# Optimization experiments

Measured on AMD Instinct MI355X. Metric: run time of the kernel, lower is better.

## Reference

```python
import jax, jax.numpy as jnp
import numpy as np
import math

B, S, E, H = 2, 2048, 1024, 16
D = E // H  # head_dim = 64


def setup_inputs() -> dict:
    key = jax.random.key(0)
    ks = jax.random.split(key, 12)
    scale = 1.0 / math.sqrt(E)
    inp = {
        "q": jax.random.normal(ks[0], (B, S, E), jnp.float32),
        "k": jax.random.normal(ks[1], (B, S, E), jnp.float32),
        "v": jax.random.normal(ks[2], (B, S, E), jnp.float32),
        # causal mask, broadcast over batch and heads
        "mask": jnp.tril(jnp.ones((S, S), jnp.bool_))[None, None, :, :],
        "Wq": jax.random.normal(ks[3], (E, E), jnp.float32) * scale,
        "bq": jnp.zeros((E,), jnp.float32),
        "Wk": jax.random.normal(ks[4], (E, E), jnp.float32) * scale,
        "bk": jnp.zeros((E,), jnp.float32),
        "Wv": jax.random.normal(ks[5], (E, E), jnp.float32) * scale,
        "bv": jnp.zeros((E,), jnp.float32),
        "Wo": jax.random.normal(ks[6], (E, E), jnp.float32) * scale,
        "bo": jnp.zeros((E,), jnp.float32),
    }
    return inp


def _heads(x, W, b):
    # nn.Linear: x @ W.T + b, then split into heads -> [B, H, S, D]
    y = x @ W.T + b
    return y.reshape(B, S, H, D).transpose(0, 2, 1, 3)


def reference(q, k, v, mask, Wq, bq, Wk, bk, Wv, bv, Wo, bo):
    qh = _heads(q, Wq, bq)   # [B,H,S,D]
    kh = _heads(k, Wk, bk)
    vh = _heads(v, Wv, bv)
    scores = jnp.einsum("bhqd,bhkd->bhqk", qh, kh) / math.sqrt(D)
    scores = jnp.where(mask, scores, -1e9)
    probs = jax.nn.softmax(scores, axis=-1)  # dropout is identity in eval
    ctx = jnp.einsum("bhqk,bhkd->bhqd", probs, vh)
    ctx = ctx.transpose(0, 2, 1, 3).reshape(B, S, E)
    return ctx @ Wo.T + bo
```

## Files before the change

### kernel.cpp

```cpp
#include <hip/hip_runtime.h>
#include <hip/hip_bf16.h>
#include <cstdint>

#define PB 2
#define PS 2048
#define PE 1024
#define PH 16
#define PD 64

typedef __attribute__((ext_vector_type(8))) short short8;
typedef __attribute__((ext_vector_type(8))) ushort u16x8;
typedef __attribute__((ext_vector_type(4))) float f32x4;

static __device__ __forceinline__ float bf2f(ushort u) {
  return __uint_as_float(((unsigned)u) << 16);
}
static __device__ __forceinline__ ushort f2bf(float f) {
  unsigned u = __float_as_uint(f);
  u += 0x7fffu + ((u >> 16) & 1u);
  return (ushort)(u >> 16);
}

static __device__ __forceinline__ void async16(void* lds, const void* g) {
  __attribute__((address_space(3))) unsigned* l =
      reinterpret_cast<__attribute__((address_space(3))) unsigned*>(
          reinterpret_cast<uintptr_t>(lds));
  const __attribute__((address_space(1))) unsigned* gp =
      reinterpret_cast<const __attribute__((address_space(1))) unsigned*>(
          reinterpret_cast<uintptr_t>(g));
  __builtin_amdgcn_global_load_lds(gp, l, 16, 0, 0);
}

__global__ __launch_bounds__(256)
void cvt_kernel(const float* __restrict__ s0, const float* __restrict__ s1,
                const float* __restrict__ s2, const float* __restrict__ s3,
                const float* __restrict__ s4, const float* __restrict__ s5,
                const float* __restrict__ s6,
                ushort* d0, ushort* d1, ushort* d2, ushort* d3, ushort* d4,
                ushort* d5, ushort* d6) {
  const int t = blockIdx.y;
  const float* src = t == 0 ? s0 : t == 1 ? s1 : t == 2 ? s2 : t == 3 ? s3
                   : t == 4 ? s4 : t == 5 ? s5 : s6;
  ushort* dst = t == 0 ? d0 : t == 1 ? d1 : t == 2 ? d2 : t == 3 ? d3
              : t == 4 ? d4 : t == 5 ? d5 : d6;
  const size_t n = (t < 3) ? (size_t)4194304 : (size_t)1048576;
  const size_t i0 = ((size_t)blockIdx.x * 256 + threadIdx.x) * 8;
  if (i0 >= n) return;
  const f32x4 a = *(const f32x4*)(src + i0);
  const f32x4 b = *(const f32x4*)(src + i0 + 4);
  u16x8 o;
  o[0] = f2bf(a[0]); o[1] = f2bf(a[1]); o[2] = f2bf(a[2]); o[3] = f2bf(a[3]);
  o[4] = f2bf(b[0]); o[5] = f2bf(b[1]); o[6] = f2bf(b[2]); o[7] = f2bf(b[3]);
  *(u16x8*)(dst + i0) = o;
}

template <bool SWAP>
__device__ __forceinline__ void gemm_core(const ushort* __restrict__ A,
                                          const ushort* __restrict__ W,
                                          int m0, int n0,
                                          ushort* As, ushort* Bs,
                                          f32x4 acc[4][4]) {
  const int tid  = threadIdx.x;
  const int wave = tid >> 6;
  const int lane = tid & 63;
  const int quad = lane >> 4;
  const int lrow = lane & 15;
  const int wm = wave >> 1;
  const int wn = wave & 1;
  const int row0 = tid >> 2;
  const int kc8  = (tid & 3) * 8;

  for (int kt = 0; kt < PE; kt += 32) {
    async16(As + (size_t)wave * 512,        A + (size_t)(m0 + row0)      * PE + kt + kc8);
    async16(As + 2048 + (size_t)wave * 512, A + (size_t)(m0 + row0 + 64) * PE + kt + kc8);
    async16(Bs + (size_t)wave * 512,        W + (size_t)(n0 + row0)      * PE + kt + kc8);
    async16(Bs + 2048 + (size_t)wave * 512, W + (size_t)(n0 + row0 + 64) * PE + kt + kc8);
    __syncthreads();
    short8 af[4], bf[4];
#pragma unroll
    for (int i = 0; i < 4; ++i) {
      af[i] = *(const short8*)(As + (wm * 64 + i * 16 + lrow) * 32 + quad * 8);
      bf[i] = *(const short8*)(Bs + (wn * 64 + i * 16 + lrow) * 32 + quad * 8);
    }
#pragma unroll
    for (int i = 0; i < 4; ++i)
#pragma unroll
      for (int j = 0; j < 4; ++j) {
        if (SWAP)
          acc[i][j] = __builtin_amdgcn_mfma_f32_16x16x32_bf16(bf[j], af[i], acc[i][j], 0, 0, 0);
        else
          acc[i][j] = __builtin_amdgcn_mfma_f32_16x16x32_bf16(af[i], bf[j], acc[i][j], 0, 0, 0);
      }
    __syncthreads();
  }
}

__global__ __launch_bounds__(256)
void qkv_kernel(const ushort* __restrict__ q, const ushort* __restrict__ k,
                const ushort* __restrict__ v,
                const ushort* __restrict__ Wq, const ushort* __restrict__ Wk,
                const ushort* __restrict__ Wv,
                const float* __restrict__ bq, const float* __restrict__ bk,
                const float* __restrict__ bv,
                ushort* __restrict__ qh, ushort* __restrict__ kh,
                ushort* __restrict__ vt) {
  __shared__ __align__(16) ushort As[128 * 32];
  __shared__ __align__(16) ushort Bs[128 * 32];
  const int which = blockIdx.x >> 3;
  const int n0 = (blockIdx.x & 7) * 128;
  const int m0 = blockIdx.y * 128;
  const ushort* A  = which == 0 ? q  : (which == 1 ? k  : v);
  const ushort* W  = which == 0 ? Wq : (which == 1 ? Wk : Wv);
  const float* bi  = which == 0 ? bq : (which == 1 ? bk : bv);

  const int lane = threadIdx.x & 63;
  const int wave = threadIdx.x >> 6;
  const int quad = lane >> 4, lrow = lane & 15;
  const int wm = wave >> 1, wn = wave & 1;

  f32x4 acc[4][4] = {};
  if (which == 2) {
    gemm_core<true>(A, W, m0, n0, As, Bs, acc);
#pragma unroll
    for (int j = 0; j < 4; ++j) {
#pragma unroll
      for (int i = 0; i < 4; ++i) {
        const int xrow = m0 + wm * 64 + i * 16 + lrow;
        const int b = xrow >> 11, s = xrow & 2047;
#pragma unroll
        for (int r = 0; r < 4; ++r) {
          const int dcol = n0 + wn * 64 + j * 16 + quad * 4 + r;
          const int h = dcol >> 6, d = dcol & 63;
          vt[((size_t)((b << 4) + h) << 17) + ((size_t)d << 11) + s] =
              f2bf(acc[i][j][r] + bi[dcol]);
        }
      }
    }
  } else {
    gemm_core<false>(A, W, m0, n0, As, Bs, acc);
    ushort* Out = which == 0 ? qh : kh;
#pragma unroll
    for (int j = 0; j < 4; ++j) {
      const int col = n0 + wn * 64 + j * 16 + lrow;
      const float bias = bi[col];
      const int h = col >> 6, d = col & 63;
#pragma unroll
      for (int i = 0; i < 4; ++i)
#pragma unroll
        for (int r = 0; r < 4; ++r) {
          const int row = m0 + wm * 64 + i * 16 + quad * 4 + r;
          const int b = row >> 11, s = row & 2047;
          Out[((size_t)((b << 4) + h) << 17) + ((size_t)s << 6) + d] =
              f2bf(acc[i][j][r] + bias);
        }
    }
  }
}

__global__ __launch_bounds__(256)
void outproj_kernel(const ushort* __restrict__ ctx, const ushort* __restrict__ Wo,
                    const float* __restrict__ bo, float* __restrict__ out) {
  __shared__ __align__(16) ushort As[128 * 32];
  __shared__ __align__(16) ushort Bs[128 * 32];
  const int n0 = blockIdx.x * 128;
  const int m0 = blockIdx.y * 128;

  f32x4 acc[4][4] = {};
  gemm_core<false>(ctx, Wo, m0, n0, As, Bs, acc);

  const int lane = threadIdx.x & 63;
  const int wave = threadIdx.x >> 6;
  const int quad = lane >> 4, lrow = lane & 15;
  const int wm = wave >> 1, wn = wave & 1;
#pragma unroll
  for (int j = 0; j < 4; ++j) {
    const int col = n0 + wn * 64 + j * 16 + lrow;
    const float bias = bo[col];
#pragma unroll
    for (int i = 0; i < 4; ++i)
#pragma unroll
      for (int r = 0; r < 4; ++r) {
        const int row = m0 + wm * 64 + i * 16 + quad * 4 + r;
        out[((size_t)row << 10) + col] = acc[i][j][r] + bias;
      }
  }
}

#define SW_IDX(r, g) (((r) << 6) + ((((g) ^ ((r) & 7))) << 3))
#define QSCALE 0.180336879f

__global__ __launch_bounds__(256)
void attn_kernel(const ushort* __restrict__ qh, const ushort* __restrict__ kh,
                 const ushort* __restrict__ vt, ushort* __restrict__ ctx) {
  __shared__ __align__(16) ushort Ks[2][4096];
  __shared__ __align__(16) ushort Vs[2][4096];
  __shared__ __align__(16) ushort Ps[4][1024];
  const int tid  = threadIdx.x;
  const int wave = tid >> 6;
  const int lane = tid & 63;
  const int quad = lane >> 4;
  const int lrow = lane & 15;
  const int bh = blockIdx.y, b = bh >> 4, h = bh & 15;
  const size_t base = (size_t)bh << 17;
  const int srow = tid >> 2;
  const int sg0  = (tid & 3) * 2;
  const int pr   = wave * 16 + lrow;
  ushort* Pw = &Ps[wave][0];
  const int prow = lrow << 6;

#pragma unroll 1
  for (int half = 0; half < 2; ++half) {
    const int qb = (half == 0) ? blockIdx.x : 31 - blockIdx.x;
    const int q0 = qb * 64;

    short8 qf0, qf1;
    {
      const ushort* qp = qh + base + (size_t)(q0 + pr) * 64 + quad * 8;
      const u16x8 a = *(const u16x8*)qp;
      const u16x8 c = *(const u16x8*)(qp + 32);
#pragma unroll
      for (int j = 0; j < 8; ++j) {
        qf0[j] = (short)f2bf(bf2f(a[j]) * QSCALE);
        qf1[j] = (short)f2bf(bf2f(c[j]) * QSCALE);
      }
    }

    f32x4 o_acc[4] = {};
    float m_i = -1e30f, l_i = 0.f;

    u16x8 kst0, kst1, vst0, vst1;
    {
      const ushort* kp = kh + base + (size_t)srow * 64 + sg0 * 8;
      kst0 = *(const u16x8*)kp; kst1 = *(const u16x8*)(kp + 8);
      const ushort* vp = vt + base + (size_t)srow * 2048 + sg0 * 8;
      vst0 = *(const u16x8*)vp; vst1 = *(const u16x8*)(vp + 8);
    }

    for (int kt = 0; kt <= qb; ++kt) {
      const int buf = kt & 1;
      *(u16x8*)&Ks[buf][SW_IDX(srow, sg0)]     = kst0;
      *(u16x8*)&Ks[buf][SW_IDX(srow, sg0 + 1)] = kst1;
      *(u16x8*)&Vs[buf][SW_IDX(srow, sg0)]     = vst0;
      *(u16x8*)&Vs[buf][SW_IDX(srow, sg0 + 1)] = vst1;
      __syncthreads();

      if (kt < qb) {
        const ushort* kp = kh + base + (size_t)((kt + 1) * 64 + srow) * 64 + sg0 * 8;
        kst0 = *(const u16x8*)kp; kst1 = *(const u16x8*)(kp + 8);
        const ushort* vp = vt + base + (size_t)srow * 2048 + (kt + 1) * 64 + sg0 * 8;
        vst0 = *(const u16x8*)vp; vst1 = *(const u16x8*)(vp + 8);
      }

      f32x4 st[4] = {};
#pragma unroll
      for (int nt = 0; nt < 4; ++nt) {
        const int r = nt * 16 + lrow;
        const short8 kb0 = *(const short8*)&Ks[buf][SW_IDX(r, quad)];
        const short8 kb1 = *(const short8*)&Ks[buf][SW_IDX(r, quad + 4)];
        st[nt] = __builtin_amdgcn_mfma_f32_16x16x32_bf16(kb0, qf0, st[nt], 0, 0, 0);
        st[nt] = __builtin_amdgcn_mfma_f32_16x16x32_bf16(kb1, qf1, st[nt], 0, 0, 0);
      }

      if (kt == qb) {
#pragma unroll
        for (int nt = 0; nt < 4; ++nt)
#pragma unroll
          for (int r = 0; r < 4; ++r)
            if (nt * 16 + quad * 4 + r > pr) st[nt][r] = -1e30f;
      }

      float rm = -1e30f;
#pragma unroll
      for (int nt = 0; nt < 4; ++nt)
#pragma unroll
        for (int r = 0; r < 4; ++r) rm = fmaxf(rm, st[nt][r]);
      rm = fmaxf(rm, __shfl_xor(rm, 16));
      rm = fmaxf(rm, __shfl_xor(rm, 32));
      const float mn = fmaxf(m_i, rm);
      const float alpha = exp2f(m_i - mn);
      m_i = mn;
      float rs = 0.f;
#pragma unroll
      for (int nt = 0; nt < 4; ++nt) {
        ushort4 pk;
        float p0 = exp2f(st[nt][0] - mn);
        float p1 = exp2f(st[nt][1] - mn);
        float p2 = exp2f(st[nt][2] - mn);
        float p3 = exp2f(st[nt][3] - mn);
        rs += (p0 + p1) + (p2 + p3);
        pk.x = f2bf(p0); pk.y = f2bf(p1); pk.z = f2bf(p2); pk.w = f2bf(p3);
        *(ushort4*)&Pw[prow + (((nt * 2 + (quad >> 1)) ^ (lrow & 7)) << 3) +
                       (quad & 1) * 4] = pk;
      }
      rs += __shfl_xor(rs, 16);
      rs += __shfl_xor(rs, 32);
      l_i = l_i * alpha + rs;
#pragma unroll
      for (int nt = 0; nt < 4; ++nt) o_acc[nt] *= alpha;

      const short8 pa0 = *(const short8*)&Pw[prow + ((quad ^ (lrow & 7)) << 3)];
      const short8 pa1 = *(const short8*)&Pw[prow + (((quad + 4) ^ (lrow & 7)) << 3)];
#pragma unroll
      for (int nt = 0; nt < 4; ++nt) {
        const int r = nt * 16 + lrow;
        const short8 vb0 = *(const short8*)&Vs[buf][SW_IDX(r, quad)];
        const short8 vb1 = *(const short8*)&Vs[buf][SW_IDX(r, quad + 4)];
        o_acc[nt] = __builtin_amdgcn_mfma_f32_16x16x32_bf16(vb0, pa0, o_acc[nt], 0, 0, 0);
        o_acc[nt] = __builtin_amdgcn_mfma_f32_16x16x32_bf16(vb1, pa1, o_acc[nt], 0, 0, 0);
      }
    }

    const float inv = 1.f / l_i;
    const size_t rowb = ((size_t)b << 21) + ((size_t)(q0 + pr) << 10) + (h << 6);
#pragma unroll
    for (int nt = 0; nt < 4; ++nt) {
      ushort4 u;
      u.x = f2bf(o_acc[nt][0] * inv);
      u.y = f2bf(o_acc[nt][1] * inv);
      u.z = f2bf(o_acc[nt][2] * inv);
      u.w = f2bf(o_acc[nt][3] * inv);
      *(ushort4*)(ctx + rowb + nt * 16 + quad * 4) = u;
    }
    __syncthreads();
  }
}

extern "C" void kernel_launch(void* const* d_in, const int* in_sizes, int n_in,
                              void* d_out, int out_size, void* d_ws, size_t ws_size,
                              hipStream_t stream) {
  const float* q  = (const float*)d_in[0];
  const float* k  = (const float*)d_in[1];
  const float* v  = (const float*)d_in[2];
  const float* Wq = (const float*)d_in[4];
  const float* bq = (const float*)d_in[5];
  const float* Wk = (const float*)d_in[6];
  const float* bk = (const float*)d_in[7];
  const float* Wv = (const float*)d_in[8];
  const float* bv = (const float*)d_in[9];
  const float* Wo = (const float*)d_in[10];
  const float* bo = (const float*)d_in[11];

  const size_t NTOK = (size_t)PB * PS * PE;
  const size_t NW   = (size_t)PE * PE;
  ushort* qh  = (ushort*)d_ws;
  ushort* kh  = qh + NTOK;
  ushort* vt  = kh + NTOK;
  ushort* qc  = vt + NTOK;
  ushort* kc  = qc + NTOK;
  ushort* vc  = kc + NTOK;
  ushort* wqc = vc + NTOK;
  ushort* wkc = wqc + NW;
  ushort* wvc = wkc + NW;
  ushort* woc = wvc + NW;
  ushort* ctx = qc;

  cvt_kernel<<<dim3(2048, 7), dim3(256), 0, stream>>>(
      q, k, v, Wq, Wk, Wv, Wo, qc, kc, vc, wqc, wkc, wvc, woc);
  qkv_kernel<<<dim3(24, 32), dim3(256), 0, stream>>>(
      qc, kc, vc, wqc, wkc, wvc, bq, bk, bv, qh, kh, vt);
  attn_kernel<<<dim3(16, 32), dim3(256), 0, stream>>>(qh, kh, vt, ctx);
  outproj_kernel<<<dim3(8, 32), dim3(256), 0, stream>>>(
      ctx, woc, bo, (float*)d_out);
}
```

Before: 254.5 us.

## Fuse activation fp32-to-bf16 conversion into QKV GEMM and split attention per q-block

The separate conversion pass over the q/k/v activations is removed. The QKV GEMM now loads fp32 activations directly and converts them to bf16 while staging them into LDS, which saves a full write and re-read of three large tensors. The attention kernel no longer pairs two query blocks per workgroup: it launches one workgroup per (batch*head, q-block), heaviest blocks first, to expose more parallelism. Packed bf16 conversion intrinsics replace the manual rounding. In exchange, the activation path no longer uses async global-to-LDS loads, and the new attention grid relies on the scheduler for load balance.

```diff
diff --git a/kernel.cpp b/kernel.cpp
--- a/kernel.cpp
+++ b/kernel.cpp
@@ -19,6 +19,16 @@
   unsigned u = __float_as_uint(f);
   u += 0x7fffu + ((u >> 16) & 1u);
   return (ushort)(u >> 16);
+}
+static __device__ __forceinline__ unsigned pkbf(float a, float b) {
+  __hip_bfloat162 h = __float22bfloat162_rn(make_float2(a, b));
+  return *reinterpret_cast<unsigned*>(&h);
+}
+static __device__ __forceinline__ u16x8 cvt8(f32x4 a, f32x4 b) {
+  union { unsigned u[4]; u16x8 v; } r;
+  r.u[0] = pkbf(a[0], a[1]); r.u[1] = pkbf(a[2], a[3]);
+  r.u[2] = pkbf(b[0], b[1]); r.u[3] = pkbf(b[2], b[3]);
+  return r.v;
 }
 
 static __device__ __forceinline__ void async16(void* lds, const void* g) {
@@ -34,24 +44,14 @@
 __global__ __launch_bounds__(256)
 void cvt_kernel(const float* __restrict__ s0, const float* __restrict__ s1,
                 const float* __restrict__ s2, const float* __restrict__ s3,
-                const float* __restrict__ s4, const float* __restrict__ s5,
-                const float* __restrict__ s6,
-                ushort* d0, ushort* d1, ushort* d2, ushort* d3, ushort* d4,
-                ushort* d5, ushort* d6) {
+                ushort* d0, ushort* d1, ushort* d2, ushort* d3) {
   const int t = blockIdx.y;
-  const float* src = t == 0 ? s0 : t == 1 ? s1 : t == 2 ? s2 : t == 3 ? s3
-                   : t == 4 ? s4 : t == 5 ? s5 : s6;
-  ushort* dst = t == 0 ? d0 : t == 1 ? d1 : t == 2 ? d2 : t == 3 ? d3
-              : t == 4 ? d4 : t == 5 ? d5 : d6;
-  const size_t n = (t < 3) ? (size_t)4194304 : (size_t)1048576;
+  const float* src = t == 0 ? s0 : t == 1 ? s1 : t == 2 ? s2 : s3;
+  ushort* dst = t == 0 ? d0 : t == 1 ? d1 : t == 2 ? d2 : d3;
   const size_t i0 = ((size_t)blockIdx.x * 256 + threadIdx.x) * 8;
-  if (i0 >= n) return;
   const f32x4 a = *(const f32x4*)(src + i0);
   const f32x4 b = *(const f32x4*)(src + i0 + 4);
-  u16x8 o;
-  o[0] = f2bf(a[0]); o[1] = f2bf(a[1]); o[2] = f2bf(a[2]); o[3] = f2bf(a[3]);
-  o[4] = f2bf(b[0]); o[5] = f2bf(b[1]); o[6] = f2bf(b[2]); o[7] = f2bf(b[3]);
-  *(u16x8*)(dst + i0) = o;
+  *(u16x8*)(dst + i0) = cvt8(a, b);
 }
 
 template <bool SWAP>
@@ -95,9 +95,54 @@
   }
 }
 
+template <bool SWAP>
+__device__ __forceinline__ void gemm_core_f32A(const float* __restrict__ A,
+                                               const ushort* __restrict__ W,
+                                               int m0, int n0,
+                                               ushort* As, ushort* Bs,
+                                               f32x4 acc[4][4]) {
+  const int tid  = threadIdx.x;
+  const int wave = tid >> 6;
+  const int lane = tid & 63;
+  const int quad = lane >> 4;
+  const int lrow = lane & 15;
+  const int wm = wave >> 1;
+  const int wn = wave & 1;
+  const int row0 = tid >> 2;
+  const int kc8  = (tid & 3) * 8;
+
+  for (int kt = 0; kt < PE; kt += 32) {
+    const float* ap0 = A + (size_t)(m0 + row0) * PE + kt + kc8;
+    const float* ap1 = A + (size_t)(m0 + row0 + 64) * PE + kt + kc8;
+    const f32x4 a0 = *(const f32x4*)ap0, a1 = *(const f32x4*)(ap0 + 4);
+    const f32x4 a2 = *(const f32x4*)ap1, a3 = *(const f32x4*)(ap1 + 4);
+    async16(Bs + (size_t)wave * 512,        W + (size_t)(n0 + row0)      * PE + kt + kc8);
+    async16(Bs + 2048 + (size_t)wave * 512, W + (size_t)(n0 + row0 + 64) * PE + kt + kc8);
+    *(u16x8*)(As + row0 * 32 + kc8)        = cvt8(a0, a1);
+    *(u16x8*)(As + (row0 + 64) * 32 + kc8) = cvt8(a2, a3);
+    __syncthreads();
+    short8 af[4], bf[4];
+#pragma unroll
+    for (int i = 0; i < 4; ++i) {
+      af[i] = *(const short8*)(As + (wm * 64 + i * 16 + lrow) * 32 + quad * 8);
+      bf[i] = *(const short8*)(Bs + (wn * 64 + i * 16 + lrow) * 32 + quad * 8);
+    }
+#pragma unroll
+    for (int i = 0; i < 4; ++i)
+#pragma unroll
+      for (int j = 0; j < 4; ++j) {
+        if (SWAP)
+          acc[i][j] = __builtin_amdgcn_mfma_f32_16x16x32_bf16(bf[j], af[i], acc[i][j], 0, 0, 0);
+        else
+          acc[i][j] = __builtin_amdgcn_mfma_f32_16x16x32_bf16(af[i], bf[j], acc[i][j], 0, 0, 0);
+      }
+    __syncthreads();
+  }
+}
+
 __global__ __launch_bounds__(256)
-void qkv_kernel(const ushort* __restrict__ q, const ushort* __restrict__ k,
-                const ushort* __restrict__ v,
+void qkv_kernel(const float* __restrict__ q, const float* __restrict__ k,
+                const float* __restrict__ v,
                 const ushort* __restrict__ Wq, const ushort* __restrict__ Wk,
                 const ushort* __restrict__ Wv,
                 const float* __restrict__ bq, const float* __restrict__ bk,
@@ -109,7 +154,7 @@
   const int which = blockIdx.x >> 3;
   const int n0 = (blockIdx.x & 7) * 128;
   const int m0 = blockIdx.y * 128;
-  const ushort* A  = which == 0 ? q  : (which == 1 ? k  : v);
+  const float* A   = which == 0 ? q  : (which == 1 ? k  : v);
   const ushort* W  = which == 0 ? Wq : (which == 1 ? Wk : Wv);
   const float* bi  = which == 0 ? bq : (which == 1 ? bk : bv);
 
@@ -120,7 +165,7 @@
 
   f32x4 acc[4][4] = {};
   if (which == 2) {
-    gemm_core<true>(A, W, m0, n0, As, Bs, acc);
+    gemm_core_f32A<true>(A, W, m0, n0, As, Bs, acc);
 #pragma unroll
     for (int j = 0; j < 4; ++j) {
 #pragma unroll
@@ -137,7 +182,7 @@
       }
     }
   } else {
-    gemm_core<false>(A, W, m0, n0, As, Bs, acc);
+    gemm_core_f32A<false>(A, W, m0, n0, As, Bs, acc);
     ushort* Out = which == 0 ? qh : kh;
 #pragma unroll
     for (int j = 0; j < 4; ++j) {
@@ -200,7 +245,7 @@
   const int lane = tid & 63;
   const int quad = lane >> 4;
   const int lrow = lane & 15;
-  const int bh = blockIdx.y, b = bh >> 4, h = bh & 15;
+  const int bh = blockIdx.x, b = bh >> 4, h = bh & 15;
   const size_t base = (size_t)bh << 17;
   const int srow = tid >> 2;
   const int sg0  = (tid & 3) * 2;
@@ -208,120 +253,114 @@
   ushort* Pw = &Ps[wave][0];
   const int prow = lrow << 6;
 
-#pragma unroll 1
-  for (int half = 0; half < 2; ++half) {
-    const int qb = (half == 0) ? blockIdx.x : 31 - blockIdx.x;
-    const int q0 = qb * 64;
-
-    short8 qf0, qf1;
-    {
-      const ushort* qp = qh + base + (size_t)(q0 + pr) * 64 + quad * 8;
-      const u16x8 a = *(const u16x8*)qp;
-      const u16x8 c = *(const u16x8*)(qp + 32);
-#pragma unroll
-      for (int j = 0; j < 8; ++j) {
-        qf0[j] = (short)f2bf(bf2f(a[j]) * QSCALE);
-        qf1[j] = (short)f2bf(bf2f(c[j]) * QSCALE);
-      }
-    }
-
-    f32x4 o_acc[4] = {};
-    float m_i = -1e30f, l_i = 0.f;
-
-    u16x8 kst0, kst1, vst0, vst1;
-    {
-      const ushort* kp = kh + base + (size_t)srow * 64 + sg0 * 8;
+  const int qb = 31 - blockIdx.y;
+  const int q0 = qb * 64;
+
+  short8 qf0, qf1;
+  {
+    const ushort* qp = qh + base + (size_t)(q0 + pr) * 64 + quad * 8;
+    const u16x8 a = *(const u16x8*)qp;
+    const u16x8 c = *(const u16x8*)(qp + 32);
+#pragma unroll
+    for (int j = 0; j < 8; ++j) {
+      qf0[j] = (short)f2bf(bf2f(a[j]) * QSCALE);
+      qf1[j] = (short)f2bf(bf2f(c[j]) * QSCALE);
+    }
+  }
+
+  f32x4 o_acc[4] = {};
+  float m_i = -1e30f, l_i = 0.f;
+
+  u16x8 kst0, kst1, vst0, vst1;
+  {
+    const ushort* kp = kh + base + (size_t)srow * 64 + sg0 * 8;
+    kst0 = *(const u16x8*)kp; kst1 = *(const u16x8*)(kp + 8);
+    const ushort* vp = vt + base + (size_t)srow * 2048 + sg0 * 8;
+    vst0 = *(const u16x8*)vp; vst1 = *(const u16x8*)(vp + 8);
+  }
+
+  for (int kt = 0; kt <= qb; ++kt) {
+    const int buf = kt & 1;
+    *(u16x8*)&Ks[buf][SW_IDX(srow, sg0)]     = kst0;
+    *(u16x8*)&Ks[buf][SW_IDX(srow, sg0 + 1)] = kst1;
+    *(u16x8*)&Vs[buf][SW_IDX(srow, sg0)]     = vst0;
+    *(u16x8*)&Vs[buf][SW_IDX(srow, sg0 + 1)] = vst1;
+    __syncthreads();
+
+    if (kt < qb) {
+      const ushort* kp = kh + base + (size_t)((kt + 1) * 64 + srow) * 64 + sg0 * 8;
       kst0 = *(const u16x8*)kp; kst1 = *(const u16x8*)(kp + 8);
-      const ushort* vp = vt + base + (size_t)srow * 2048 + sg0 * 8;
+      const ushort* vp = vt + base + (size_t)srow * 2048 + (kt + 1) * 64 + sg0 * 8;
       vst0 = *(const u16x8*)vp; vst1 = *(const u16x8*)(vp + 8);
     }
 
-    for (int kt = 0; kt <= qb; ++kt) {
-      const int buf = kt & 1;
-      *(u16x8*)&Ks[buf][SW_IDX(srow, sg0)]     = kst0;
-      *(u16x8*)&Ks[buf][SW_IDX(srow, sg0 + 1)] = kst1;
-      *(u16x8*)&Vs[buf][SW_IDX(srow, sg0)]     = vst0;
-      *(u16x8*)&Vs[buf][SW_IDX(srow, sg0 + 1)] = vst1;
-      __syncthreads();
-
-      if (kt < qb) {
-        const ushort* kp = kh + base + (size_t)((kt + 1) * 64 + srow) * 64 + sg0 * 8;
-        kst0 = *(const u16x8*)kp; kst1 = *(const u16x8*)(kp + 8);
-        const ushort* vp = vt + base + (size_t)srow * 2048 + (kt + 1) * 64 + sg0 * 8;
-        vst0 = *(const u16x8*)vp; vst1 = *(const u16x8*)(vp + 8);
-      }
-
-      f32x4 st[4] = {};
-#pragma unroll
-      for (int nt = 0; nt < 4; ++nt) {
-        const int r = nt * 16 + lrow;
-        const short8 kb0 = *(const short8*)&Ks[buf][SW_IDX(r, quad)];
-        const short8 kb1 = *(const short8*)&Ks[buf][SW_IDX(r, quad + 4)];
-        st[nt] = __builtin_amdgcn_mfma_f32_16x16x32_bf16(kb0, qf0, st[nt], 0, 0, 0);
-        st[nt] = __builtin_amdgcn_mfma_f32_16x16x32_bf16(kb1, qf1, st[nt], 0, 0, 0);
-      }
-
-      if (kt == qb) {
-#pragma unroll
-        for (int nt = 0; nt < 4; ++nt)
-#pragma unroll
-          for (int r = 0; r < 4; ++r)
-            if (nt * 16 + quad * 4 + r > pr) st[nt][r] = -1e30f;
-      }
-
-      float rm = -1e30f;
+    f32x4 st[4] = {};
+#pragma unroll
+    for (int nt = 0; nt < 4; ++nt) {
+      const int r = nt * 16 + lrow;
+      const short8 kb0 = *(const short8*)&Ks[buf][SW_IDX(r, quad)];
+      const short8 kb1 = *(const short8*)&Ks[buf][SW_IDX(r, quad + 4)];
+      st[nt] = __builtin_amdgcn_mfma_f32_16x16x32_bf16(kb0, qf0, st[nt], 0, 0, 0);
+      st[nt] = __builtin_amdgcn_mfma_f32_16x16x32_bf16(kb1, qf1, st[nt], 0, 0, 0);
+    }
+
+    if (kt == qb) {
 #pragma unroll
       for (int nt = 0; nt < 4; ++nt)
 #pragma unroll
-        for (int r = 0; r < 4; ++r) rm = fmaxf(rm, st[nt][r]);
-      rm = fmaxf(rm, __shfl_xor(rm, 16));
-      rm = fmaxf(rm, __shfl_xor(rm, 32));
-      const float mn = fmaxf(m_i, rm);
-      const float alpha = exp2f(m_i - mn);
-      m_i = mn;
-      float rs = 0.f;
-#pragma unroll
-      for (int nt = 0; nt < 4; ++nt) {
-        ushort4 pk;
-        float p0 = exp2f(st[nt][0] - mn);
-        float p1 = exp2f(st[nt][1] - mn);
-        float p2 = exp2f(st[nt][2] - mn);
-        float p3 = exp2f(st[nt][3] - mn);
-        rs += (p0 + p1) + (p2 + p3);
-        pk.x = f2bf(p0); pk.y = f2bf(p1); pk.z = f2bf(p2); pk.w = f2bf(p3);
-        *(ushort4*)&Pw[prow + (((nt * 2 + (quad >> 1)) ^ (lrow & 7)) << 3) +
-                       (quad & 1) * 4] = pk;
-      }
-      rs += __shfl_xor(rs, 16);
-      rs += __shfl_xor(rs, 32);
-      l_i = l_i * alpha + rs;
-#pragma unroll
-      for (int nt = 0; nt < 4; ++nt) o_acc[nt] *= alpha;
-
-      const short8 pa0 = *(const short8*)&Pw[prow + ((quad ^ (lrow & 7)) << 3)];
-      const short8 pa1 = *(const short8*)&Pw[prow + (((quad + 4) ^ (lrow & 7)) << 3)];
-#pragma unroll
-      for (int nt = 0; nt < 4; ++nt) {
-        const int r = nt * 16 + lrow;
-        const short8 vb0 = *(const short8*)&Vs[buf][SW_IDX(r, quad)];
-        const short8 vb1 = *(const short8*)&Vs[buf][SW_IDX(r, quad + 4)];
-        o_acc[nt] = __builtin_amdgcn_mfma_f32_16x16x32_bf16(vb0, pa0, o_acc[nt], 0, 0, 0);
-        o_acc[nt] = __builtin_amdgcn_mfma_f32_16x16x32_bf16(vb1, pa1, o_acc[nt], 0, 0, 0);
-      }
-    }
-
-    const float inv = 1.f / l_i;
-    const size_t rowb = ((size_t)b << 21) + ((size_t)(q0 + pr) << 10) + (h << 6);
+        for (int r = 0; r < 4; ++r)
+          if (nt * 16 + quad * 4 + r > pr) st[nt][r] = -1e30f;
+    }
+
+    float rm = -1e30f;
+#pragma unroll
+    for (int nt = 0; nt < 4; ++nt)
+#pragma unroll
+      for (int r = 0; r < 4; ++r) rm = fmaxf(rm, st[nt][r]);
+    rm = fmaxf(rm, __shfl_xor(rm, 16));
+    rm = fmaxf(rm, __shfl_xor(rm, 32));
+    const float mn = fmaxf(m_i, rm);
+    const float alpha = exp2f(m_i - mn);
+    m_i = mn;
+    float rs = 0.f;
 #pragma unroll
     for (int nt = 0; nt < 4; ++nt) {
-      ushort4 u;
-      u.x = f2bf(o_acc[nt][0] * inv);
-      u.y = f2bf(o_acc[nt][1] * inv);
-      u.z = f2bf(o_acc[nt][2] * inv);
-      u.w = f2bf(o_acc[nt][3] * inv);
-      *(ushort4*)(ctx + rowb + nt * 16 + quad * 4) = u;
-    }
-    __syncthreads();
+      float p0 = exp2f(st[nt][0] - mn);
+      float p1 = exp2f(st[nt][1] - mn);
+      float p2 = exp2f(st[nt][2] - mn);
+      float p3 = exp2f(st[nt][3] - mn);
+      rs += (p0 + p1) + (p2 + p3);
+      uint2 pk;
+      pk.x = pkbf(p0, p1); pk.y = pkbf(p2, p3);
+      *(uint2*)&Pw[prow + (((nt * 2 + (quad >> 1)) ^ (lrow & 7)) << 3) +
+                   (quad & 1) * 4] = pk;
+    }
+    rs += __shfl_xor(rs, 16);
+    rs += __shfl_xor(rs, 32);
+    l_i = l_i * alpha + rs;
+#pragma unroll
+    for (int nt = 0; nt < 4; ++nt) o_acc[nt] *= alpha;
+
+    const short8 pa0 = *(const short8*)&Pw[prow + ((quad ^ (lrow & 7)) << 3)];
+    const short8 pa1 = *(const short8*)&Pw[prow + (((quad + 4) ^ (lrow & 7)) << 3)];
+#pragma unroll
+    for (int nt = 0; nt < 4; ++nt) {
+      const int r = nt * 16 + lrow;
+      const short8 vb0 = *(const short8*)&Vs[buf][SW_IDX(r, quad)];
+      const short8 vb1 = *(const short8*)&Vs[buf][SW_IDX(r, quad + 4)];
+      o_acc[nt] = __builtin_amdgcn_mfma_f32_16x16x32_bf16(vb0, pa0, o_acc[nt], 0, 0, 0);
+      o_acc[nt] = __builtin_amdgcn_mfma_f32_16x16x32_bf16(vb1, pa1, o_acc[nt], 0, 0, 0);
+    }
+  }
+
+  const float inv = 1.f / l_i;
+  const size_t rowb = ((size_t)b << 21) + ((size_t)(q0 + pr) << 10) + (h << 6);
+#pragma unroll
+  for (int nt = 0; nt < 4; ++nt) {
+    uint2 u;
+    u.x = pkbf(o_acc[nt][0] * inv, o_acc[nt][1] * inv);
+    u.y = pkbf(o_acc[nt][2] * inv, o_acc[nt][3] * inv);
+    *(uint2*)(ctx + rowb + nt * 16 + quad * 4) = u;
   }
 }
 
@@ -345,20 +384,17 @@
   ushort* qh  = (ushort*)d_ws;
   ushort* kh  = qh + NTOK;
   ushort* vt  = kh + NTOK;
-  ushort* qc  = vt + NTOK;
-  ushort* kc  = qc + NTOK;
-  ushort* vc  = kc + NTOK;
-  ushort* wqc = vc + NTOK;
+  ushort* ctx = vt + NTOK;
+  ushort* wqc = ctx + NTOK;
   ushort* wkc = wqc + NW;
   ushort* wvc = wkc + NW;
   ushort* woc = wvc + NW;
-  ushort* ctx = qc;
-
-  cvt_kernel<<<dim3(2048, 7), dim3(256), 0, stream>>>(
-      q, k, v, Wq, Wk, Wv, Wo, qc, kc, vc, wqc, wkc, wvc, woc);
+
+  cvt_kernel<<<dim3(512, 4), dim3(256), 0, stream>>>(
+      Wq, Wk, Wv, Wo, wqc, wkc, wvc, woc);
   qkv_kernel<<<dim3(24, 32), dim3(256), 0, stream>>>(
-      qc, kc, vc, wqc, wkc, wvc, bq, bk, bv, qh, kh, vt);
-  attn_kernel<<<dim3(16, 32), dim3(256), 0, stream>>>(qh, kh, vt, ctx);
+      q, k, v, wqc, wkc, wvc, bq, bk, bv, qh, kh, vt);
+  attn_kernel<<<dim3(32, 32), dim3(256), 0, stream>>>(qh, kh, vt, ctx);
   outproj_kernel<<<dim3(8, 32), dim3(256), 0, stream>>>(
       ctx, woc, bo, (float*)d_out);
 }
```

Measured after the change: 275.8 us. 1.08x slower.

## Split attention into one block per query tile, longest first; reorder grids; packed bf16 converts

Applied to the files above, without the earlier changes.

The attention kernel no longer pairs a short and a long query tile inside one block. It now launches 1024 blocks, one per (batch-head, query tile), ordered so the longest causal tiles dispatch first, which aims to improve load balancing and occupancy. The QKV and output-projection grids are transposed so that consecutive blocks share the same weight columns. Scalar bf16 rounding is replaced with packed float2-to-bf16x2 conversions in the cast, softmax-P and output stores. In exchange, the split launches more blocks that each reload their own Q tile, and the new tail depends on how the hardware schedules the short tiles.

```diff
diff --git a/kernel.cpp b/kernel.cpp
--- a/kernel.cpp
+++ b/kernel.cpp
@@ -19,6 +19,16 @@
   unsigned u = __float_as_uint(f);
   u += 0x7fffu + ((u >> 16) & 1u);
   return (ushort)(u >> 16);
+}
+static __device__ __forceinline__ unsigned pkbf(float a, float b) {
+  __hip_bfloat162 h = __float22bfloat162_rn(make_float2(a, b));
+  return *reinterpret_cast<unsigned*>(&h);
+}
+static __device__ __forceinline__ u16x8 cvt8(f32x4 a, f32x4 b) {
+  union { unsigned u[4]; u16x8 v; } r;
+  r.u[0] = pkbf(a[0], a[1]); r.u[1] = pkbf(a[2], a[3]);
+  r.u[2] = pkbf(b[0], b[1]); r.u[3] = pkbf(b[2], b[3]);
+  return r.v;
 }
 
 static __device__ __forceinline__ void async16(void* lds, const void* g) {
@@ -48,10 +58,7 @@
   if (i0 >= n) return;
   const f32x4 a = *(const f32x4*)(src + i0);
   const f32x4 b = *(const f32x4*)(src + i0 + 4);
-  u16x8 o;
-  o[0] = f2bf(a[0]); o[1] = f2bf(a[1]); o[2] = f2bf(a[2]); o[3] = f2bf(a[3]);
-  o[4] = f2bf(b[0]); o[5] = f2bf(b[1]); o[6] = f2bf(b[2]); o[7] = f2bf(b[3]);
-  *(u16x8*)(dst + i0) = o;
+  *(u16x8*)(dst + i0) = cvt8(a, b);
 }
 
 template <bool SWAP>
@@ -106,9 +113,9 @@
                 ushort* __restrict__ vt) {
   __shared__ __align__(16) ushort As[128 * 32];
   __shared__ __align__(16) ushort Bs[128 * 32];
-  const int which = blockIdx.x >> 3;
-  const int n0 = (blockIdx.x & 7) * 128;
-  const int m0 = blockIdx.y * 128;
+  const int which = blockIdx.y >> 3;
+  const int n0 = (blockIdx.y & 7) * 128;
+  const int m0 = blockIdx.x * 128;
   const ushort* A  = which == 0 ? q  : (which == 1 ? k  : v);
   const ushort* W  = which == 0 ? Wq : (which == 1 ? Wk : Wv);
   const float* bi  = which == 0 ? bq : (which == 1 ? bk : bv);
@@ -162,8 +169,8 @@
                     const float* __restrict__ bo, float* __restrict__ out) {
   __shared__ __align__(16) ushort As[128 * 32];
   __shared__ __align__(16) ushort Bs[128 * 32];
-  const int n0 = blockIdx.x * 128;
-  const int m0 = blockIdx.y * 128;
+  const int n0 = blockIdx.y * 128;
+  const int m0 = blockIdx.x * 128;
 
   f32x4 acc[4][4] = {};
   gemm_core<false>(ctx, Wo, m0, n0, As, Bs, acc);
@@ -200,7 +207,7 @@
   const int lane = tid & 63;
   const int quad = lane >> 4;
   const int lrow = lane & 15;
-  const int bh = blockIdx.y, b = bh >> 4, h = bh & 15;
+  const int bh = blockIdx.x, b = bh >> 4, h = bh & 15;
   const size_t base = (size_t)bh << 17;
   const int srow = tid >> 2;
   const int sg0  = (tid & 3) * 2;
@@ -208,120 +215,114 @@
   ushort* Pw = &Ps[wave][0];
   const int prow = lrow << 6;
 
-#pragma unroll 1
-  for (int half = 0; half < 2; ++half) {
-    const int qb = (half == 0) ? blockIdx.x : 31 - blockIdx.x;
-    const int q0 = qb * 64;
-
-    short8 qf0, qf1;
-    {
-      const ushort* qp = qh + base + (size_t)(q0 + pr) * 64 + quad * 8;
-      const u16x8 a = *(const u16x8*)qp;
-      const u16x8 c = *(const u16x8*)(qp + 32);
-#pragma unroll
-      for (int j = 0; j < 8; ++j) {
-        qf0[j] = (short)f2bf(bf2f(a[j]) * QSCALE);
-        qf1[j] = (short)f2bf(bf2f(c[j]) * QSCALE);
-      }
-    }
-
-    f32x4 o_acc[4] = {};
-    float m_i = -1e30f, l_i = 0.f;
-
-    u16x8 kst0, kst1, vst0, vst1;
-    {
-      const ushort* kp = kh + base + (size_t)srow * 64 + sg0 * 8;
+  const int qb = 31 - blockIdx.y;
+  const int q0 = qb * 64;
+
+  short8 qf0, qf1;
+  {
+    const ushort* qp = qh + base + (size_t)(q0 + pr) * 64 + quad * 8;
+    const u16x8 a = *(const u16x8*)qp;
+    const u16x8 c = *(const u16x8*)(qp + 32);
+#pragma unroll
+    for (int j = 0; j < 8; ++j) {
+      qf0[j] = (short)f2bf(bf2f(a[j]) * QSCALE);
+      qf1[j] = (short)f2bf(bf2f(c[j]) * QSCALE);
+    }
+  }
+
+  f32x4 o_acc[4] = {};
+  float m_i = -1e30f, l_i = 0.f;
+
+  u16x8 kst0, kst1, vst0, vst1;
+  {
+    const ushort* kp = kh + base + (size_t)srow * 64 + sg0 * 8;
+    kst0 = *(const u16x8*)kp; kst1 = *(const u16x8*)(kp + 8);
+    const ushort* vp = vt + base + (size_t)srow * 2048 + sg0 * 8;
+    vst0 = *(const u16x8*)vp; vst1 = *(const u16x8*)(vp + 8);
+  }
+
+  for (int kt = 0; kt <= qb; ++kt) {
+    const int buf = kt & 1;
+    *(u16x8*)&Ks[buf][SW_IDX(srow, sg0)]     = kst0;
+    *(u16x8*)&Ks[buf][SW_IDX(srow, sg0 + 1)] = kst1;
+    *(u16x8*)&Vs[buf][SW_IDX(srow, sg0)]     = vst0;
+    *(u16x8*)&Vs[buf][SW_IDX(srow, sg0 + 1)] = vst1;
+    __syncthreads();
+
+    if (kt < qb) {
+      const ushort* kp = kh + base + (size_t)((kt + 1) * 64 + srow) * 64 + sg0 * 8;
       kst0 = *(const u16x8*)kp; kst1 = *(const u16x8*)(kp + 8);
-      const ushort* vp = vt + base + (size_t)srow * 2048 + sg0 * 8;
+      const ushort* vp = vt + base + (size_t)srow * 2048 + (kt + 1) * 64 + sg0 * 8;
       vst0 = *(const u16x8*)vp; vst1 = *(const u16x8*)(vp + 8);
     }
 
-    for (int kt = 0; kt <= qb; ++kt) {
-      const int buf = kt & 1;
-      *(u16x8*)&Ks[buf][SW_IDX(srow, sg0)]     = kst0;
-      *(u16x8*)&Ks[buf][SW_IDX(srow, sg0 + 1)] = kst1;
-      *(u16x8*)&Vs[buf][SW_IDX(srow, sg0)]     = vst0;
-      *(u16x8*)&Vs[buf][SW_IDX(srow, sg0 + 1)] = vst1;
-      __syncthreads();
-
-      if (kt < qb) {
-        const ushort* kp = kh + base + (size_t)((kt + 1) * 64 + srow) * 64 + sg0 * 8;
-        kst0 = *(const u16x8*)kp; kst1 = *(const u16x8*)(kp + 8);
-        const ushort* vp = vt + base + (size_t)srow * 2048 + (kt + 1) * 64 + sg0 * 8;
-        vst0 = *(const u16x8*)vp; vst1 = *(const u16x8*)(vp + 8);
-      }
-
-      f32x4 st[4] = {};
-#pragma unroll
-      for (int nt = 0; nt < 4; ++nt) {
-        const int r = nt * 16 + lrow;
-        const short8 kb0 = *(const short8*)&Ks[buf][SW_IDX(r, quad)];
-        const short8 kb1 = *(const short8*)&Ks[buf][SW_IDX(r, quad + 4)];
-        st[nt] = __builtin_amdgcn_mfma_f32_16x16x32_bf16(kb0, qf0, st[nt], 0, 0, 0);
-        st[nt] = __builtin_amdgcn_mfma_f32_16x16x32_bf16(kb1, qf1, st[nt], 0, 0, 0);
-      }
-
-      if (kt == qb) {
-#pragma unroll
-        for (int nt = 0; nt < 4; ++nt)
-#pragma unroll
-          for (int r = 0; r < 4; ++r)
-            if (nt * 16 + quad * 4 + r > pr) st[nt][r] = -1e30f;
-      }
-
-      float rm = -1e30f;
+    f32x4 st[4] = {};
+#pragma unroll
+    for (int nt = 0; nt < 4; ++nt) {
+      const int r = nt * 16 + lrow;
+      const short8 kb0 = *(const short8*)&Ks[buf][SW_IDX(r, quad)];
+      const short8 kb1 = *(const short8*)&Ks[buf][SW_IDX(r, quad + 4)];
+      st[nt] = __builtin_amdgcn_mfma_f32_16x16x32_bf16(kb0, qf0, st[nt], 0, 0, 0);
+      st[nt] = __builtin_amdgcn_mfma_f32_16x16x32_bf16(kb1, qf1, st[nt], 0, 0, 0);
+    }
+
+    if (kt == qb) {
 #pragma unroll
       for (int nt = 0; nt < 4; ++nt)
 #pragma unroll
-        for (int r = 0; r < 4; ++r) rm = fmaxf(rm, st[nt][r]);
-      rm = fmaxf(rm, __shfl_xor(rm, 16));
-      rm = fmaxf(rm, __shfl_xor(rm, 32));
-      const float mn = fmaxf(m_i, rm);
-      const float alpha = exp2f(m_i - mn);
-      m_i = mn;
-      float rs = 0.f;
-#pragma unroll
-      for (int nt = 0; nt < 4; ++nt) {
-        ushort4 pk;
-        float p0 = exp2f(st[nt][0] - mn);
-        float p1 = exp2f(st[nt][1] - mn);
-        float p2 = exp2f(st[nt][2] - mn);
-        float p3 = exp2f(st[nt][3] - mn);
-        rs += (p0 + p1) + (p2 + p3);
-        pk.x = f2bf(p0); pk.y = f2bf(p1); pk.z = f2bf(p2); pk.w = f2bf(p3);
-        *(ushort4*)&Pw[prow + (((nt * 2 + (quad >> 1)) ^ (lrow & 7)) << 3) +
-                       (quad & 1) * 4] = pk;
-      }
-      rs += __shfl_xor(rs, 16);
-      rs += __shfl_xor(rs, 32);
-      l_i = l_i * alpha + rs;
-#pragma unroll
-      for (int nt = 0; nt < 4; ++nt) o_acc[nt] *= alpha;
-
-      const short8 pa0 = *(const short8*)&Pw[prow + ((quad ^ (lrow & 7)) << 3)];
-      const short8 pa1 = *(const short8*)&Pw[prow + (((quad + 4) ^ (lrow & 7)) << 3)];
-#pragma unroll
-      for (int nt = 0; nt < 4; ++nt) {
-        const int r = nt * 16 + lrow;
-        const short8 vb0 = *(const short8*)&Vs[buf][SW_IDX(r, quad)];
-        const short8 vb1 = *(const short8*)&Vs[buf][SW_IDX(r, quad + 4)];
-        o_acc[nt] = __builtin_amdgcn_mfma_f32_16x16x32_bf16(vb0, pa0, o_acc[nt], 0, 0, 0);
-        o_acc[nt] = __builtin_amdgcn_mfma_f32_16x16x32_bf16(vb1, pa1, o_acc[nt], 0, 0, 0);
-      }
-    }
-
-    const float inv = 1.f / l_i;
-    const size_t rowb = ((size_t)b << 21) + ((size_t)(q0 + pr) << 10) + (h << 6);
+        for (int r = 0; r < 4; ++r)
+          if (nt * 16 + quad * 4 + r > pr) st[nt][r] = -1e30f;
+    }
+
+    float rm = -1e30f;
+#pragma unroll
+    for (int nt = 0; nt < 4; ++nt)
+#pragma unroll
+      for (int r = 0; r < 4; ++r) rm = fmaxf(rm, st[nt][r]);
+    rm = fmaxf(rm, __shfl_xor(rm, 16));
+    rm = fmaxf(rm, __shfl_xor(rm, 32));
+    const float mn = fmaxf(m_i, rm);
+    const float alpha = exp2f(m_i - mn);
+    m_i = mn;
+    float rs = 0.f;
 #pragma unroll
     for (int nt = 0; nt < 4; ++nt) {
-      ushort4 u;
-      u.x = f2bf(o_acc[nt][0] * inv);
-      u.y = f2bf(o_acc[nt][1] * inv);
-      u.z = f2bf(o_acc[nt][2] * inv);
-      u.w = f2bf(o_acc[nt][3] * inv);
-      *(ushort4*)(ctx + rowb + nt * 16 + quad * 4) = u;
-    }
-    __syncthreads();
+      float p0 = exp2f(st[nt][0] - mn);
+      float p1 = exp2f(st[nt][1] - mn);
+      float p2 = exp2f(st[nt][2] - mn);
+      float p3 = exp2f(st[nt][3] - mn);
+      rs += (p0 + p1) + (p2 + p3);
+      uint2 pk;
+      pk.x = pkbf(p0, p1); pk.y = pkbf(p2, p3);
+      *(uint2*)&Pw[prow + (((nt * 2 + (quad >> 1)) ^ (lrow & 7)) << 3) +
+                   (quad & 1) * 4] = pk;
+    }
+    rs += __shfl_xor(rs, 16);
+    rs += __shfl_xor(rs, 32);
+    l_i = l_i * alpha + rs;
+#pragma unroll
+    for (int nt = 0; nt < 4; ++nt) o_acc[nt] *= alpha;
+
+    const short8 pa0 = *(const short8*)&Pw[prow + ((quad ^ (lrow & 7)) << 3)];
+    const short8 pa1 = *(const short8*)&Pw[prow + (((quad + 4) ^ (lrow & 7)) << 3)];
+#pragma unroll
+    for (int nt = 0; nt < 4; ++nt) {
+      const int r = nt * 16 + lrow;
+      const short8 vb0 = *(const short8*)&Vs[buf][SW_IDX(r, quad)];
+      const short8 vb1 = *(const short8*)&Vs[buf][SW_IDX(r, quad + 4)];
+      o_acc[nt] = __builtin_amdgcn_mfma_f32_16x16x32_bf16(vb0, pa0, o_acc[nt], 0, 0, 0);
+      o_acc[nt] = __builtin_amdgcn_mfma_f32_16x16x32_bf16(vb1, pa1, o_acc[nt], 0, 0, 0);
+    }
+  }
+
+  const float inv = 1.f / l_i;
+  const size_t rowb = ((size_t)b << 21) + ((size_t)(q0 + pr) << 10) + (h << 6);
+#pragma unroll
+  for (int nt = 0; nt < 4; ++nt) {
+    uint2 u;
+    u.x = pkbf(o_acc[nt][0] * inv, o_acc[nt][1] * inv);
+    u.y = pkbf(o_acc[nt][2] * inv, o_acc[nt][3] * inv);
+    *(uint2*)(ctx + rowb + nt * 16 + quad * 4) = u;
   }
 }
 
@@ -356,9 +357,9 @@
 
   cvt_kernel<<<dim3(2048, 7), dim3(256), 0, stream>>>(
       q, k, v, Wq, Wk, Wv, Wo, qc, kc, vc, wqc, wkc, wvc, woc);
-  qkv_kernel<<<dim3(24, 32), dim3(256), 0, stream>>>(
+  qkv_kernel<<<dim3(32, 24), dim3(256), 0, stream>>>(
       qc, kc, vc, wqc, wkc, wvc, bq, bk, bv, qh, kh, vt);
-  attn_kernel<<<dim3(16, 32), dim3(256), 0, stream>>>(qh, kh, vt, ctx);
-  outproj_kernel<<<dim3(8, 32), dim3(256), 0, stream>>>(
+  attn_kernel<<<dim3(32, 32), dim3(256), 0, stream>>>(qh, kh, vt, ctx);
+  outproj_kernel<<<dim3(32, 8), dim3(256), 0, stream>>>(
       ctx, woc, bo, (float*)d_out);
 }
```

Result: faster. 240.6 us (-5.5%).
